# Kernel tuning notes

Measured on AMD Instinct MI355X. Metric: run time of the kernel, lower is better.

The kernel has to match this reference:

```python
import jax, jax.numpy as jnp
import numpy as np

N, E, D, H, DH, FF, C, L = 50000, 640000, 128, 8, 16, 256, 5, 6
EPS = 1e-5


def _bn(x, g, b):
    # training-mode BatchNorm1d over the node dimension
    m = jnp.mean(x, axis=0)
    v = jnp.var(x, axis=0)
    return (x - m) * jax.lax.rsqrt(v + EPS) * g + b


def _sparse_mha(x, src, dst, Wq, Wk, Wv, Wo):
    # edge-restricted multi-head attention: softmax over incoming edges per dst node
    q = (x @ Wq).reshape(N, H, DH)
    k = (x @ Wk).reshape(N, H, DH)
    v = (x @ Wv).reshape(N, H, DH)
    s = jnp.einsum('ehd,ehd->eh', q[dst], k[src]) * (1.0 / np.sqrt(DH))  # [E,H]
    smax = jax.ops.segment_max(s, dst, num_segments=N)
    smax = jnp.where(jnp.isfinite(smax), smax, 0.0)  # guard isolated nodes
    e = jnp.exp(s - smax[dst])
    den = jax.ops.segment_sum(e, dst, num_segments=N)
    alpha = e / jnp.where(den > 0, den, 1.0)[dst]
    out = jax.ops.segment_sum(alpha[:, :, None] * v[src], dst, num_segments=N)  # [N,H,DH]
    return out.reshape(N, D) @ Wo


def setup_inputs() -> dict:
    key = jax.random.key(0)
    ks = jax.random.split(key, 18)
    f = lambda k, shp, sc: (jax.random.normal(k, shp, jnp.float32) * sc)
    return {
        'x': jax.random.normal(ks[0], (N, D), jnp.float32),
        'edge_index': jax.random.randint(ks[1], (2, E), 0, N),
        'Wq': f(ks[2], (L, D, D), 0.08),
        'Wk': f(ks[3], (L, D, D), 0.08),
        'Wv': f(ks[4], (L, D, D), 0.08),
        'Wo': f(ks[5], (L, D, D), 0.08),
        'g1': jnp.ones((L, D), jnp.float32),
        'bn1': jnp.zeros((L, D), jnp.float32),
        'W1': f(ks[6], (L, D, FF), 0.08),
        'bf1': jnp.zeros((L, FF), jnp.float32),
        'W2': f(ks[7], (L, FF, D), 0.06),
        'bf2': jnp.zeros((L, D), jnp.float32),
        'g2': jnp.ones((L, D), jnp.float32),
        'bn2': jnp.zeros((L, D), jnp.float32),
        'Wp': f(ks[8], (D, C), 0.08),
        'bp': jnp.zeros((C,), jnp.float32),
    }


def reference(x, edge_index, Wq, Wk, Wv, Wo, g1, bn1, W1, bf1, W2, bf2, g2, bn2, Wp, bp):
    src, dst = edge_index[0], edge_index[1]
    for i in range(L):  # fixed small layer count
        res = x  # residual is Identity (num_input == num_output)
        a = _sparse_mha(x, src, dst, Wq[i], Wk[i], Wv[i], Wo[i])
        x = _bn(a + res, g1[i], bn1[i])
        h = jax.nn.relu(x @ W1[i] + bf1[i])  # leakiness=0 -> relu
        x = _bn(x + (h @ W2[i] + bf2[i]), g2[i], bn2[i])
    node_pred = x @ Wp + bp
    return node_pred
```

## Files before the change

### kernel.cpp

```cpp
#include <hip/hip_runtime.h>
#include <hip/hip_bf16.h>
#include <cstdio>

#define NN 50000
#define EE 640000
#define DD 128
#define HH 8
#define DH 16
#define FFD 256
#define CC 5
#define LL 6
#define EPSV 1e-5f

typedef __attribute__((ext_vector_type(8))) short bf16x8;
typedef __attribute__((ext_vector_type(8))) unsigned short ushort8;
typedef __attribute__((ext_vector_type(4))) float f32x4;

__device__ __forceinline__ float bfu2f(unsigned short u) {
  union { unsigned int i; float f; } x; x.i = ((unsigned int)u) << 16; return x.f;
}
__device__ __forceinline__ unsigned short f2bf(float f) {
  union { float f; unsigned int i; } x; x.f = f;
  unsigned int r = (x.i + 0x7fffu + ((x.i >> 16) & 1u)) >> 16;
  return (unsigned short)r;
}

__global__ void detect_kernel(const unsigned int* __restrict__ g1w, int* __restrict__ flag) {
  if (threadIdx.x == 0 && blockIdx.x == 0) *flag = (g1w[0] == 0x3F803F80u) ? 1 : 0;
}

struct ConvJobs { const void* in[8]; float* out[8]; int n[8]; };
__global__ __launch_bounds__(256) void convert_batch_kernel(ConvJobs jobs, const int* __restrict__ flag) {
  int b = blockIdx.x;
  const void* in = jobs.in[b];
  float* out = jobs.out[b];
  int n = jobs.n[b];
  int use_bf = *flag;
  for (int i = threadIdx.x; i < n; i += 256) {
    if (use_bf) out[i] = bfu2f(((const unsigned short*)in)[i]);
    else        out[i] = ((const float*)in)[i];
  }
}

__global__ __launch_bounds__(256) void to_bf16_kernel(const void* __restrict__ in,
                                                      unsigned short* __restrict__ out, int n,
                                                      const int* __restrict__ flag) {
  int i = blockIdx.x * blockDim.x + threadIdx.x;
  if (i >= n) return;
  if (*flag) out[i] = ((const unsigned short*)in)[i];
  else       out[i] = f2bf(((const float*)in)[i]);
}

__global__ __launch_bounds__(256) void t_qkv_kernel(const void* __restrict__ wq, const void* __restrict__ wk,
                                                    const void* __restrict__ wv,
                                                    unsigned short* __restrict__ qkvT,
                                                    const int* __restrict__ flag) {
  int k = blockIdx.x, which = blockIdx.y, l = blockIdx.z;
  const void* in = (which == 0) ? wq : (which == 1) ? wk : wv;
  size_t off = (size_t)l * DD * DD;
  unsigned short* out = qkvT + (size_t)l * 384 * DD + (size_t)which * DD * DD;
  int use_bf = *flag;
  for (int n = threadIdx.x; n < DD; n += 256) {
    unsigned short v;
    if (use_bf) v = ((const unsigned short*)in)[off + (size_t)k * DD + n];
    else        v = f2bf(((const float*)in)[off + (size_t)k * DD + n]);
    out[(size_t)n * DD + k] = v;
  }
}

__global__ __launch_bounds__(256) void t_w_kernel(const void* __restrict__ in,
                                                  unsigned short* __restrict__ out,
                                                  int K, int N, const int* __restrict__ flag) {
  int k = blockIdx.x, l = blockIdx.y;
  size_t off = (size_t)l * K * N;
  unsigned short* o = out + (size_t)l * K * N;
  int use_bf = *flag;
  for (int n = threadIdx.x; n < N; n += 256) {
    unsigned short v;
    if (use_bf) v = ((const unsigned short*)in)[off + (size_t)k * N + n];
    else        v = f2bf(((const float*)in)[off + (size_t)k * N + n]);
    o[(size_t)n * K + k] = v;
  }
}

__global__ __launch_bounds__(256) void zero_kernel(int* __restrict__ p, int n) {
  int i = blockIdx.x * blockDim.x + threadIdx.x;
  if (i < n) p[i] = 0;
}

__global__ __launch_bounds__(256) void count_kernel(const int* __restrict__ dst, int* __restrict__ counts) {
  int e = blockIdx.x * blockDim.x + threadIdx.x;
  if (e < EE) atomicAdd(&counts[dst[e]], 1);
}

__global__ __launch_bounds__(256) void scan1_kernel(const int* __restrict__ counts,
                                                    int* __restrict__ row_ptr, int* __restrict__ partials) {
  __shared__ int sh[256];
  int t = threadIdx.x;
  int i = blockIdx.x * 256 + t;
  int v = (i < NN) ? counts[i] : 0;
  sh[t] = v; __syncthreads();
#pragma unroll
  for (int off = 1; off < 256; off <<= 1) {
    int u = (t >= off) ? sh[t - off] : 0;
    __syncthreads();
    sh[t] += u;
    __syncthreads();
  }
  if (i < NN) row_ptr[i] = sh[t] - v;
  if (t == 255) partials[blockIdx.x] = sh[t];
}

__global__ __launch_bounds__(256) void scan2_kernel(int* __restrict__ partials, int nb) {
  __shared__ int sh[256];
  int t = threadIdx.x;
  int v = (t < nb) ? partials[t] : 0;
  sh[t] = v; __syncthreads();
#pragma unroll
  for (int off = 1; off < 256; off <<= 1) {
    int u = (t >= off) ? sh[t - off] : 0;
    __syncthreads();
    sh[t] += u;
    __syncthreads();
  }
  if (t < nb) partials[t] = sh[t] - v;
}

__global__ __launch_bounds__(256) void scan3_kernel(int* __restrict__ row_ptr, const int* __restrict__ partials) {
  int i = blockIdx.x * 256 + threadIdx.x;
  if (i < NN) row_ptr[i] += partials[blockIdx.x];
  if (i == 0) row_ptr[NN] = EE;
}

__global__ __launch_bounds__(256) void fill_kernel(const int* __restrict__ src, const int* __restrict__ dst,
                                                   const int* __restrict__ row_ptr, int* __restrict__ cursor,
                                                   int* __restrict__ csr_src) {
  int e = blockIdx.x * blockDim.x + threadIdx.x;
  if (e < EE) {
    int d = dst[e];
    int pos = row_ptr[d] + atomicAdd(&cursor[d], 1);
    csr_src[pos] = src[e];
  }
}

template<int K, bool RELU, bool HASBIAS, bool HASRES, bool OUTBF, bool STATS>
__global__ __launch_bounds__(256) void mfma_gemm(const unsigned short* __restrict__ A,
                                                 const unsigned short* __restrict__ BT,
                                                 const float* __restrict__ bias,
                                                 const unsigned short* __restrict__ resid,
                                                 void* __restrict__ C, float* __restrict__ stats,
                                                 int M, int ldc) {
  __shared__ float lsum[64];
  __shared__ float lsq[64];
  int tid = threadIdx.x;
  int lane = tid & 63, wave = tid >> 6;
  int m0 = blockIdx.x * 128 + wave * 32;
  int n0 = blockIdx.y * 64;
  int lm = lane & 15;
  int quad = lane >> 4;
  int kq = quad * 8;

  int rowA[2];
#pragma unroll
  for (int r = 0; r < 2; r++) {
    int rr = m0 + 16 * r + lm;
    rowA[r] = (rr < M) ? rr : (M - 1);
  }
  const unsigned short* aptr0 = A + (size_t)rowA[0] * K + kq;
  const unsigned short* aptr1 = A + (size_t)rowA[1] * K + kq;
  const unsigned short* bptr[4];
#pragma unroll
  for (int c = 0; c < 4; c++)
    bptr[c] = BT + (size_t)(n0 + 16 * c + lm) * K + kq;

  f32x4 acc[2][4];
#pragma unroll
  for (int r = 0; r < 2; r++)
#pragma unroll
    for (int c = 0; c < 4; c++) acc[r][c] = (f32x4){0.f, 0.f, 0.f, 0.f};

#pragma unroll
  for (int kc = 0; kc < K; kc += 128) {
    bf16x8 a[2][4], b[4][4];
#pragma unroll
    for (int ks = 0; ks < 4; ks++) {
      a[0][ks] = *(const bf16x8*)(aptr0 + kc + ks * 32);
      a[1][ks] = *(const bf16x8*)(aptr1 + kc + ks * 32);
    }
#pragma unroll
    for (int c = 0; c < 4; c++)
#pragma unroll
      for (int ks = 0; ks < 4; ks++)
        b[c][ks] = *(const bf16x8*)(bptr[c] + kc + ks * 32);
#pragma unroll
    for (int ks = 0; ks < 4; ks++)
#pragma unroll
      for (int r = 0; r < 2; r++)
#pragma unroll
        for (int c = 0; c < 4; c++)
          acc[r][c] = __builtin_amdgcn_mfma_f32_16x16x32_bf16(a[r][ks], b[c][ks], acc[r][c], 0, 0, 0);
  }

  if (STATS) {
    if (tid < 64) { lsum[tid] = 0.f; lsq[tid] = 0.f; }
    __syncthreads();
  }

#pragma unroll
  for (int c = 0; c < 4; c++) {
    int col = n0 + 16 * c + lm;
    float bv = HASBIAS ? bias[col] : 0.f;
    float ps = 0.f, pss = 0.f;
#pragma unroll
    for (int r = 0; r < 2; r++) {
#pragma unroll
      for (int reg = 0; reg < 4; reg++) {
        int row = m0 + 16 * r + quad * 4 + reg;
        if (row < M) {
          float o = acc[r][c][reg] + bv;
          if (HASRES) o += bfu2f(resid[(size_t)row * ldc + col]);
          if (RELU) o = fmaxf(o, 0.f);
          size_t idx = (size_t)row * ldc + col;
          if (OUTBF) ((unsigned short*)C)[idx] = f2bf(o);
          else       ((float*)C)[idx] = o;
          if (STATS) { ps += o; pss = fmaf(o, o, pss); }
        }
      }
    }
    if (STATS) {
      atomicAdd(&lsum[16 * c + lm], ps);
      atomicAdd(&lsq[16 * c + lm], pss);
    }
  }
  if (STATS) {
    __syncthreads();
    if (tid < 64) {
      atomicAdd(&stats[n0 + tid], lsum[tid]);
      atomicAdd(&stats[128 + n0 + tid], lsq[tid]);
    }
  }
}

__global__ __launch_bounds__(256) void attn_kernel(const unsigned short* __restrict__ qkv,
                                                   const int* __restrict__ row_ptr,
                                                   const int* __restrict__ csr_src,
                                                   unsigned short* __restrict__ t1) {
  int t = blockIdx.x * blockDim.x + threadIdx.x;
  if (t >= NN * HH) return;
  int n = t >> 3, h = t & 7;
  const unsigned short* qp = qkv + (size_t)n * 384 + h * 16;
  float qf[16];
  {
    bf16x8 q0 = *(const bf16x8*)qp;
    bf16x8 q1 = *(const bf16x8*)(qp + 8);
#pragma unroll
    for (int i = 0; i < 8; i++) { qf[i] = bfu2f((unsigned short)q0[i]); qf[8 + i] = bfu2f((unsigned short)q1[i]); }
  }
  float m = -3.0e38f, l = 0.f;
  float A[16];
#pragma unroll
  for (int i = 0; i < 16; i++) A[i] = 0.f;
  int e0 = row_ptr[n], e1 = row_ptr[n + 1];
  if (e0 < e1) {
    int s = csr_src[e0];
    const unsigned short* kp = qkv + (size_t)s * 384 + 128 + h * 16;
    bf16x8 k0 = *(const bf16x8*)kp;
    bf16x8 k1 = *(const bf16x8*)(kp + 8);
    bf16x8 v0 = *(const bf16x8*)(kp + 128);
    bf16x8 v1 = *(const bf16x8*)(kp + 136);
    for (int e = e0; e < e1; e++) {
      int sn = csr_src[(e + 1 < e1) ? e + 1 : e];
      const unsigned short* kpn = qkv + (size_t)sn * 384 + 128 + h * 16;
      bf16x8 nk0 = *(const bf16x8*)kpn;
      bf16x8 nk1 = *(const bf16x8*)(kpn + 8);
      bf16x8 nv0 = *(const bf16x8*)(kpn + 128);
      bf16x8 nv1 = *(const bf16x8*)(kpn + 136);

      float sc = 0.f;
#pragma unroll
      for (int i = 0; i < 8; i++) {
        sc += qf[i] * bfu2f((unsigned short)k0[i]);
        sc += qf[8 + i] * bfu2f((unsigned short)k1[i]);
      }
      sc *= 0.25f;
      float mn = fmaxf(m, sc);
      float cf = __expf(m - mn);
      float p  = __expf(sc - mn);
      l = l * cf + p;
#pragma unroll
      for (int i = 0; i < 8; i++) {
        A[i]     = A[i]     * cf + p * bfu2f((unsigned short)v0[i]);
        A[8 + i] = A[8 + i] * cf + p * bfu2f((unsigned short)v1[i]);
      }
      m = mn;
      k0 = nk0; k1 = nk1; v0 = nv0; v1 = nv1;
    }
  }
  float inv = (l > 0.f) ? 1.f / l : 0.f;
  ushort8 o0, o1;
#pragma unroll
  for (int i = 0; i < 8; i++) { o0[i] = f2bf(A[i] * inv); o1[i] = f2bf(A[8 + i] * inv); }
  unsigned short* op = t1 + (size_t)n * 128 + h * 16;
  *(ushort8*)op = o0;
  *(ushort8*)(op + 8) = o1;
}

__global__ __launch_bounds__(256) void bn_apply_kernel(const float4* __restrict__ y4,
                                                       const float* __restrict__ statsL,
                                                       const float* __restrict__ g,
                                                       const float* __restrict__ b,
                                                       ushort4* __restrict__ xb) {
  __shared__ float ssc[128];
  __shared__ float ssh[128];
  int t = threadIdx.x;
  if (t < 128) {
    float mean = statsL[t] * (1.f / NN);
    float var  = statsL[128 + t] * (1.f / NN) - mean * mean;
    var = fmaxf(var, 0.f);
    float sc = g[t] * rsqrtf(var + EPSV);
    ssc[t] = sc;
    ssh[t] = b[t] - mean * sc;
  }
  __syncthreads();
  int i = blockIdx.x * 256 + t;
  const int total = NN * (DD / 4);
  if (i >= total) return;
  int c4 = (i & 31) * 4;
  float4 v = y4[i];
  ushort4 o;
  o.x = f2bf(fmaf(v.x, ssc[c4 + 0], ssh[c4 + 0]));
  o.y = f2bf(fmaf(v.y, ssc[c4 + 1], ssh[c4 + 1]));
  o.z = f2bf(fmaf(v.z, ssc[c4 + 2], ssh[c4 + 2]));
  o.w = f2bf(fmaf(v.w, ssc[c4 + 3], ssh[c4 + 3]));
  xb[i] = o;
}

__global__ __launch_bounds__(256) void proj_kernel(const unsigned short* __restrict__ x,
                                                   const float* __restrict__ Wp,
                                                   const float* __restrict__ bp,
                                                   void* __restrict__ out,
                                                   const int* __restrict__ flag) {
  __shared__ float W[DD * CC];
  __shared__ float bias[CC];
  for (int i = threadIdx.x; i < DD * CC; i += 256) W[i] = Wp[i];
  if (threadIdx.x < CC) bias[threadIdx.x] = bp[threadIdx.x];
  __syncthreads();
  int n = blockIdx.x * blockDim.x + threadIdx.x;
  if (n >= NN) return;
  float acc[CC];
#pragma unroll
  for (int c = 0; c < CC; c++) acc[c] = bias[c];
  const ushort4* xp = (const ushort4*)(x + (size_t)n * DD);
#pragma unroll
  for (int k4 = 0; k4 < DD / 4; k4++) {
    ushort4 u = xp[k4];
    float a0 = bfu2f(u.x), a1 = bfu2f(u.y), a2 = bfu2f(u.z), a3 = bfu2f(u.w);
    const float* w = &W[k4 * 4 * CC];
#pragma unroll
    for (int c = 0; c < CC; c++)
      acc[c] += a0 * w[c] + a1 * w[CC + c] + a2 * w[2 * CC + c] + a3 * w[3 * CC + c];
  }
  if (*flag) {
    __hip_bfloat16* o16 = (__hip_bfloat16*)out;
#pragma unroll
    for (int c = 0; c < CC; c++) o16[(size_t)n * CC + c] = __float2bfloat16(acc[c]);
  } else {
    float* o32 = (float*)out;
#pragma unroll
    for (int c = 0; c < CC; c++) o32[(size_t)n * CC + c] = acc[c];
  }
}

extern "C" void kernel_launch(void* const* d_in, const int* in_sizes, int n_in,
                              void* d_out, int out_size, void* d_ws, size_t ws_size,
                              hipStream_t stream) {
  const int* ei = (const int*)d_in[1];

  char* p = (char*)d_ws;
  auto carve = [&](size_t bytes) { char* r = p; p += (bytes + 255) & ~(size_t)255; return (void*)r; };
  unsigned short* xb   = (unsigned short*)carve((size_t)NN * DD * 2);
  unsigned short* qkv  = (unsigned short*)carve((size_t)NN * 384 * 2);
  unsigned short* t1   = (unsigned short*)carve((size_t)NN * DD * 2);
  unsigned short* hbuf = (unsigned short*)carve((size_t)NN * FFD * 2);
  float* y             = (float*)carve((size_t)NN * DD * 4);
  float* stats = (float*)carve(12 * 256 * 4);
  int* row_ptr = (int*)carve((size_t)(NN + 1) * 4);
  int* cursor  = (int*)carve((size_t)NN * 4);
  int* counts  = (int*)carve((size_t)NN * 4);
  int* csr_src = (int*)carve((size_t)EE * 4);
  int* flag    = (int*)carve(256);
  int* partials = (int*)carve(256 * 4);
  unsigned short* qkvT = (unsigned short*)carve((size_t)LL * 384 * DD * 2);
  unsigned short* WoT  = (unsigned short*)carve((size_t)LL * DD * DD * 2);
  unsigned short* W1T  = (unsigned short*)carve((size_t)LL * FFD * DD * 2);
  unsigned short* W2T  = (unsigned short*)carve((size_t)LL * DD * FFD * 2);
  float* g1_f  = (float*)carve((size_t)LL * DD * 4);
  float* bn1_f = (float*)carve((size_t)LL * DD * 4);
  float* bf1_f = (float*)carve((size_t)LL * FFD * 4);
  float* bf2_f = (float*)carve((size_t)LL * DD * 4);
  float* g2_f  = (float*)carve((size_t)LL * DD * 4);
  float* bn2_f = (float*)carve((size_t)LL * DD * 4);
  float* Wp_f  = (float*)carve((size_t)DD * CC * 4);
  float* bp_f  = (float*)carve((size_t)CC * 4);
  size_t need = (size_t)(p - (char*)d_ws);
  if (need > ws_size) {
    fprintf(stderr, "kernel_launch: workspace too small: need %zu, have %zu\n", need, ws_size);
    return;
  }

  const int* src  = ei;
  const int* dstp = ei + EE;

  detect_kernel<<<1, 64, 0, stream>>>((const unsigned int*)d_in[6], flag);
  to_bf16_kernel<<<(NN * DD + 255) / 256, 256, 0, stream>>>(d_in[0], xb, NN * DD, flag);

  {
    ConvJobs j;
    j.in[0] = d_in[6];  j.out[0] = g1_f;  j.n[0] = LL * DD;
    j.in[1] = d_in[7];  j.out[1] = bn1_f; j.n[1] = LL * DD;
    j.in[2] = d_in[9];  j.out[2] = bf1_f; j.n[2] = LL * FFD;
    j.in[3] = d_in[11]; j.out[3] = bf2_f; j.n[3] = LL * DD;
    j.in[4] = d_in[12]; j.out[4] = g2_f;  j.n[4] = LL * DD;
    j.in[5] = d_in[13]; j.out[5] = bn2_f; j.n[5] = LL * DD;
    j.in[6] = d_in[14]; j.out[6] = Wp_f;  j.n[6] = DD * CC;
    j.in[7] = d_in[15]; j.out[7] = bp_f;  j.n[7] = CC;
    convert_batch_kernel<<<8, 256, 0, stream>>>(j, flag);
  }

  t_qkv_kernel<<<dim3(DD, 3, LL), 256, 0, stream>>>(d_in[2], d_in[3], d_in[4], qkvT, flag);
  t_w_kernel<<<dim3(DD, LL), 256, 0, stream>>>(d_in[5], WoT, DD, DD, flag);
  t_w_kernel<<<dim3(DD, LL), 256, 0, stream>>>(d_in[8], W1T, DD, FFD, flag);
  t_w_kernel<<<dim3(FFD, LL), 256, 0, stream>>>(d_in[10], W2T, FFD, DD, flag);

  zero_kernel<<<12, 256, 0, stream>>>((int*)stats, 12 * 256);
  zero_kernel<<<(NN + 255) / 256, 256, 0, stream>>>(counts, NN);
  zero_kernel<<<(NN + 255) / 256, 256, 0, stream>>>(cursor, NN);

  const int NB = (NN + 255) / 256;
  count_kernel<<<(EE + 255) / 256, 256, 0, stream>>>(dstp, counts);
  scan1_kernel<<<NB, 256, 0, stream>>>(counts, row_ptr, partials);
  scan2_kernel<<<1, 256, 0, stream>>>(partials, NB);
  scan3_kernel<<<NB, 256, 0, stream>>>(row_ptr, partials);
  fill_kernel<<<(EE + 255) / 256, 256, 0, stream>>>(src, dstp, row_ptr, cursor, csr_src);

  const int gm = (NN + 127) / 128;
  for (int layer = 0; layer < LL; layer++) {
    const unsigned short* qkvT_l = qkvT + (size_t)layer * 384 * DD;
    const unsigned short* WoT_l  = WoT  + (size_t)layer * DD * DD;
    const unsigned short* W1T_l  = W1T  + (size_t)layer * FFD * DD;
    const unsigned short* W2T_l  = W2T  + (size_t)layer * DD * FFD;
    float* st1 = stats + (size_t)(layer * 2 + 0) * 256;
    float* st2 = stats + (size_t)(layer * 2 + 1) * 256;

    mfma_gemm<128, false, false, false, true, false><<<dim3(gm, 6), 256, 0, stream>>>(
        xb, qkvT_l, nullptr, nullptr, qkv, nullptr, NN, 384);
    attn_kernel<<<(NN * HH + 255) / 256, 256, 0, stream>>>(qkv, row_ptr, csr_src, t1);
    mfma_gemm<128, false, false, true, false, true><<<dim3(gm, 2), 256, 0, stream>>>(
        t1, WoT_l, nullptr, xb, y, st1, NN, 128);
    bn_apply_kernel<<<(NN * 32 + 255) / 256, 256, 0, stream>>>(
        (const float4*)y, st1, g1_f + (size_t)layer * DD, bn1_f + (size_t)layer * DD, (ushort4*)xb);

    mfma_gemm<128, true, true, false, true, false><<<dim3(gm, 4), 256, 0, stream>>>(
        xb, W1T_l, bf1_f + (size_t)layer * FFD, nullptr, hbuf, nullptr, NN, 256);
    mfma_gemm<256, false, true, true, false, true><<<dim3(gm, 2), 256, 0, stream>>>(
        hbuf, W2T_l, bf2_f + (size_t)layer * DD, xb, y, st2, NN, 128);
    bn_apply_kernel<<<(NN * 32 + 255) / 256, 256, 0, stream>>>(
        (const float4*)y, st2, g2_f + (size_t)layer * DD, bn2_f + (size_t)layer * DD, (ushort4*)xb);
  }

  proj_kernel<<<(NN + 255) / 256, 256, 0, stream>>>(xb, Wp_f, bp_f, d_out, flag);
}
```

Baseline: 1.488 ms.

## Split attention head across two lanes and vectorize GEMM epilogue via transposed MFMA

The attention kernel now uses two threads per (node, head), each holding 8 of the 16 head dims and combining partial dot products with a lane shuffle. This doubles thread count and halves registers per thread, giving more memory-level parallelism for the gathers. Separately, the MFMA operands are swapped so each lane holds 4 consecutive columns, which lets the GEMM epilogue use vectorized float4/ushort4 loads and stores. BN statistics are then reduced with cross-lane shuffles before the shared-memory atomics, which cuts the atomic count. The attention grid drops the bounds check and assumes NN*HH*2 is divisible by 256, which holds for these sizes.

```diff
diff --git a/kernel.cpp b/kernel.cpp
--- a/kernel.cpp
+++ b/kernel.cpp
@@ -198,7 +198,7 @@
       for (int r = 0; r < 2; r++)
 #pragma unroll
         for (int c = 0; c < 4; c++)
-          acc[r][c] = __builtin_amdgcn_mfma_f32_16x16x32_bf16(a[r][ks], b[c][ks], acc[r][c], 0, 0, 0);
+          acc[r][c] = __builtin_amdgcn_mfma_f32_16x16x32_bf16(b[c][ks], a[r][ks], acc[r][c], 0, 0, 0);
   }
 
   if (STATS) {
@@ -206,33 +206,66 @@
     __syncthreads();
   }
 
-#pragma unroll
-  for (int c = 0; c < 4; c++) {
-    int col = n0 + 16 * c + lm;
-    float bv = HASBIAS ? bias[col] : 0.f;
-    float ps = 0.f, pss = 0.f;
-#pragma unroll
-    for (int r = 0; r < 2; r++) {
-#pragma unroll
-      for (int reg = 0; reg < 4; reg++) {
-        int row = m0 + 16 * r + quad * 4 + reg;
-        if (row < M) {
-          float o = acc[r][c][reg] + bv;
-          if (HASRES) o += bfu2f(resid[(size_t)row * ldc + col]);
-          if (RELU) o = fmaxf(o, 0.f);
-          size_t idx = (size_t)row * ldc + col;
-          if (OUTBF) ((unsigned short*)C)[idx] = f2bf(o);
-          else       ((float*)C)[idx] = o;
-          if (STATS) { ps += o; pss = fmaf(o, o, pss); }
+  float st_s[4][4], st_q[4][4];
+  if (STATS) {
+#pragma unroll
+    for (int c = 0; c < 4; c++)
+#pragma unroll
+      for (int reg = 0; reg < 4; reg++) { st_s[c][reg] = 0.f; st_q[c][reg] = 0.f; }
+  }
+
+#pragma unroll
+  for (int r = 0; r < 2; r++) {
+    int row = m0 + 16 * r + lm;
+    if (row >= M) continue;
+#pragma unroll
+    for (int c = 0; c < 4; c++) {
+      int col = n0 + 16 * c + quad * 4;
+      float4 bv = HASBIAS ? *(const float4*)(bias + col) : make_float4(0.f, 0.f, 0.f, 0.f);
+      float o[4];
+      o[0] = acc[r][c][0] + bv.x; o[1] = acc[r][c][1] + bv.y;
+      o[2] = acc[r][c][2] + bv.z; o[3] = acc[r][c][3] + bv.w;
+      if (HASRES) {
+        ushort4 rr = *(const ushort4*)(resid + (size_t)row * ldc + col);
+        o[0] += bfu2f(rr.x); o[1] += bfu2f(rr.y); o[2] += bfu2f(rr.z); o[3] += bfu2f(rr.w);
+      }
+      if (RELU) {
+        o[0] = fmaxf(o[0], 0.f); o[1] = fmaxf(o[1], 0.f);
+        o[2] = fmaxf(o[2], 0.f); o[3] = fmaxf(o[3], 0.f);
+      }
+      size_t idx = (size_t)row * ldc + col;
+      if (OUTBF) {
+        ushort4 w;
+        w.x = f2bf(o[0]); w.y = f2bf(o[1]); w.z = f2bf(o[2]); w.w = f2bf(o[3]);
+        *(ushort4*)((unsigned short*)C + idx) = w;
+      } else {
+        *(float4*)((float*)C + idx) = make_float4(o[0], o[1], o[2], o[3]);
+      }
+      if (STATS) {
+#pragma unroll
+        for (int reg = 0; reg < 4; reg++) {
+          st_s[c][reg] += o[reg];
+          st_q[c][reg] = fmaf(o[reg], o[reg], st_q[c][reg]);
         }
       }
     }
-    if (STATS) {
-      atomicAdd(&lsum[16 * c + lm], ps);
-      atomicAdd(&lsq[16 * c + lm], pss);
-    }
-  }
+  }
+
   if (STATS) {
+#pragma unroll
+    for (int c = 0; c < 4; c++)
+#pragma unroll
+      for (int reg = 0; reg < 4; reg++) {
+        float s = st_s[c][reg], q = st_q[c][reg];
+        s += __shfl_xor(s, 1);  q += __shfl_xor(q, 1);
+        s += __shfl_xor(s, 2);  q += __shfl_xor(q, 2);
+        s += __shfl_xor(s, 4);  q += __shfl_xor(q, 4);
+        s += __shfl_xor(s, 8);  q += __shfl_xor(q, 8);
+        if (lm == 0) {
+          atomicAdd(&lsum[16 * c + quad * 4 + reg], s);
+          atomicAdd(&lsq[16 * c + quad * 4 + reg], q);
+        }
+      }
     __syncthreads();
     if (tid < 64) {
       atomicAdd(&stats[n0 + tid], lsum[tid]);
@@ -246,63 +279,53 @@
                                                    const int* __restrict__ csr_src,
                                                    unsigned short* __restrict__ t1) {
   int t = blockIdx.x * blockDim.x + threadIdx.x;
-  if (t >= NN * HH) return;
-  int n = t >> 3, h = t & 7;
-  const unsigned short* qp = qkv + (size_t)n * 384 + h * 16;
-  float qf[16];
+  int half = t & 1;
+  int nh = t >> 1;
+  int n = nh >> 3, h = nh & 7;
+  const unsigned short* qp = qkv + (size_t)n * 384 + h * 16 + half * 8;
+  float qf[8];
   {
     bf16x8 q0 = *(const bf16x8*)qp;
-    bf16x8 q1 = *(const bf16x8*)(qp + 8);
-#pragma unroll
-    for (int i = 0; i < 8; i++) { qf[i] = bfu2f((unsigned short)q0[i]); qf[8 + i] = bfu2f((unsigned short)q1[i]); }
+#pragma unroll
+    for (int i = 0; i < 8; i++) qf[i] = bfu2f((unsigned short)q0[i]);
   }
   float m = -3.0e38f, l = 0.f;
-  float A[16];
-#pragma unroll
-  for (int i = 0; i < 16; i++) A[i] = 0.f;
+  float A[8];
+#pragma unroll
+  for (int i = 0; i < 8; i++) A[i] = 0.f;
   int e0 = row_ptr[n], e1 = row_ptr[n + 1];
   if (e0 < e1) {
     int s = csr_src[e0];
-    const unsigned short* kp = qkv + (size_t)s * 384 + 128 + h * 16;
+    const unsigned short* kp = qkv + (size_t)s * 384 + 128 + h * 16 + half * 8;
     bf16x8 k0 = *(const bf16x8*)kp;
-    bf16x8 k1 = *(const bf16x8*)(kp + 8);
     bf16x8 v0 = *(const bf16x8*)(kp + 128);
-    bf16x8 v1 = *(const bf16x8*)(kp + 136);
     for (int e = e0; e < e1; e++) {
       int sn = csr_src[(e + 1 < e1) ? e + 1 : e];
-      const unsigned short* kpn = qkv + (size_t)sn * 384 + 128 + h * 16;
+      const unsigned short* kpn = qkv + (size_t)sn * 384 + 128 + h * 16 + half * 8;
       bf16x8 nk0 = *(const bf16x8*)kpn;
-      bf16x8 nk1 = *(const bf16x8*)(kpn + 8);
       bf16x8 nv0 = *(const bf16x8*)(kpn + 128);
-      bf16x8 nv1 = *(const bf16x8*)(kpn + 136);
-
-      float sc = 0.f;
-#pragma unroll
-      for (int i = 0; i < 8; i++) {
-        sc += qf[i] * bfu2f((unsigned short)k0[i]);
-        sc += qf[8 + i] * bfu2f((unsigned short)k1[i]);
-      }
-      sc *= 0.25f;
+
+      float part = 0.f;
+#pragma unroll
+      for (int i = 0; i < 8; i++) part += qf[i] * bfu2f((unsigned short)k0[i]);
+      float sc = (part + __shfl_xor(part, 1)) * 0.25f;
       float mn = fmaxf(m, sc);
       float cf = __expf(m - mn);
       float p  = __expf(sc - mn);
       l = l * cf + p;
 #pragma unroll
-      for (int i = 0; i < 8; i++) {
-        A[i]     = A[i]     * cf + p * bfu2f((unsigned short)v0[i]);
-        A[8 + i] = A[8 + i] * cf + p * bfu2f((unsigned short)v1[i]);
-      }
+      for (int i = 0; i < 8; i++)
+        A[i] = A[i] * cf + p * bfu2f((unsigned short)v0[i]);
       m = mn;
-      k0 = nk0; k1 = nk1; v0 = nv0; v1 = nv1;
+      k0 = nk0; v0 = nv0;
     }
   }
   float inv = (l > 0.f) ? 1.f / l : 0.f;
-  ushort8 o0, o1;
-#pragma unroll
-  for (int i = 0; i < 8; i++) { o0[i] = f2bf(A[i] * inv); o1[i] = f2bf(A[8 + i] * inv); }
-  unsigned short* op = t1 + (size_t)n * 128 + h * 16;
+  ushort8 o0;
+#pragma unroll
+  for (int i = 0; i < 8; i++) o0[i] = f2bf(A[i] * inv);
+  unsigned short* op = t1 + (size_t)n * 128 + h * 16 + half * 8;
   *(ushort8*)op = o0;
-  *(ushort8*)(op + 8) = o1;
 }
 
 __global__ __launch_bounds__(256) void bn_apply_kernel(const float4* __restrict__ y4,
@@ -454,7 +477,7 @@
 
     mfma_gemm<128, false, false, false, true, false><<<dim3(gm, 6), 256, 0, stream>>>(
         xb, qkvT_l, nullptr, nullptr, qkv, nullptr, NN, 384);
-    attn_kernel<<<(NN * HH + 255) / 256, 256, 0, stream>>>(qkv, row_ptr, csr_src, t1);
+    attn_kernel<<<NN * HH * 2 / 256, 256, 0, stream>>>(qkv, row_ptr, csr_src, t1);
     mfma_gemm<128, false, false, true, false, true><<<dim3(gm, 2), 256, 0, stream>>>(
         t1, WoT_l, nullptr, xb, y, st1, NN, 128);
     bn_apply_kernel<<<(NN * 32 + 255) / 256, 256, 0, stream>>>(
```

New measurement: 1.424 ms. 4.3% less time.
